# Performance work log

Measured on AMD Instinct MI355X. Metric: run time of the kernel, lower is better.

The kernel has to match this reference:

```python
import jax, jax.numpy as jnp
import numpy as np

D_MODEL = 2048
N_HEADS = 32
N_KV = 8
HEAD_DIM = D_MODEL // N_HEADS  # 64
ROPE_BASE = 500000.0


def _rope_tables(seq_len, dim, dtype):
    inv_freq = 1.0 / (ROPE_BASE ** (jnp.arange(0, dim, 2, dtype=jnp.float32) / dim))
    t = jnp.arange(seq_len, dtype=jnp.float32)
    freqs = jnp.outer(t, inv_freq)          # [S, dim/2]
    emb = jnp.concatenate([freqs, freqs], axis=-1)  # [S, dim]
    return jnp.cos(emb).astype(dtype), jnp.sin(emb).astype(dtype)


def _rotate_half(x):
    x1, x2 = jnp.split(x, 2, axis=-1)
    return jnp.concatenate([-x2, x1], axis=-1)


def setup_inputs() -> dict:
    key = jax.random.key(0)
    ks = jax.random.split(key, 5)
    B, S = 2, 2048
    sc = 0.02
    return {
        "x": jax.random.normal(ks[0], (B, S, D_MODEL), jnp.float32),
        "Wq": jax.random.normal(ks[1], (D_MODEL, N_HEADS * HEAD_DIM), jnp.float32) * sc,
        "Wk": jax.random.normal(ks[2], (D_MODEL, N_KV * HEAD_DIM), jnp.float32) * sc,
        "Wv": jax.random.normal(ks[3], (D_MODEL, N_KV * HEAD_DIM), jnp.float32) * sc,
        "Wo": jax.random.normal(ks[4], (N_HEADS * HEAD_DIM, D_MODEL), jnp.float32) * sc,
    }


def reference(x, Wq, Wk, Wv, Wo):
    B, S, _ = x.shape
    n_rep = N_HEADS // N_KV

    q = (x @ Wq).reshape(B, S, N_HEADS, HEAD_DIM)
    k = (x @ Wk).reshape(B, S, N_KV, HEAD_DIM)
    v = (x @ Wv).reshape(B, S, N_KV, HEAD_DIM)

    cos, sin = _rope_tables(S, HEAD_DIM, x.dtype)
    cos = cos[None, :, None, :]  # [1,S,1,D]
    sin = sin[None, :, None, :]
    q = q * cos + _rotate_half(q) * sin
    k = k * cos + _rotate_half(k) * sin

    # GQA without materializing expanded K/V: group q heads by kv head.
    qg = q.reshape(B, S, N_KV, n_rep, HEAD_DIM)
    scale = 1.0 / jnp.sqrt(jnp.asarray(HEAD_DIM, x.dtype))
    # scores: [B, n_kv, n_rep, Sq, Sk]
    scores = jnp.einsum("bqhrd,bkhd->bhrqk", qg, k) * scale
    attn = jax.nn.softmax(scores, axis=-1)
    out = jnp.einsum("bhrqk,bkhd->bqhrd", attn, v)  # [B,S,n_kv,n_rep,D]
    out = out.reshape(B, S, N_HEADS * HEAD_DIM)
    return out @ Wo
```

## Files before the change

### kernel.cpp

```cpp
#include <hip/hip_runtime.h>
#include <hip/hip_bf16.h>
#include <stdint.h>

#define SS    2048
#define BB    2
#define MT    4096
#define DM    2048
#define NQKVC 3072

typedef __attribute__((ext_vector_type(8))) short s16x8;
typedef __attribute__((ext_vector_type(4))) short s16x4;
typedef __attribute__((ext_vector_type(4))) float f32x4;
typedef __attribute__((ext_vector_type(2))) unsigned u32x2;

typedef __attribute__((address_space(1))) const void* as1cv;
typedef __attribute__((address_space(3))) void* as3v;

__device__ __forceinline__ float b2f(int u) {
  union { unsigned u; float f; } x; x.u = ((unsigned)(u & 0xFFFF)) << 16; return x.f;
}
__device__ __forceinline__ short f2b(float f) {
  union { float f; unsigned u; } x; x.f = f;
  unsigned r = x.u + 0x7FFFu + ((x.u >> 16) & 1u);
  return (short)(r >> 16);
}
__device__ __forceinline__ void gld16(const void* g, void* l) {
  __builtin_amdgcn_global_load_lds((as1cv)(uintptr_t)g, (as3v)(uint32_t)(uintptr_t)l, 16, 0, 0);
}
__device__ __forceinline__ s16x8 ldsfrag(const char* tile, int r, int cb) {
  return *(const s16x8*)(tile + r * 128 + (cb ^ ((r & 7) << 4)));
}
__device__ __forceinline__ f32x4 mfma16(s16x8 a, s16x8 b, f32x4 c) {
  return __builtin_amdgcn_mfma_f32_16x16x32_bf16(a, b, c, 0, 0, 0);
}

__global__ __launch_bounds__(256) void k_xcvt(const float* __restrict__ x,
                                              ushort* __restrict__ xb, int n) {
  int i = (blockIdx.x * 256 + threadIdx.x) * 4;
  if (i >= n) return;
  float4 v = *(const float4*)(x + i);
  s16x4 o = { f2b(v.x), f2b(v.y), f2b(v.z), f2b(v.w) };
  *(s16x4*)(xb + i) = o;
}

__global__ __launch_bounds__(256) void k_rtab(float* __restrict__ rtab) {
  int idx = blockIdx.x * 256 + threadIdx.x;
  int d = idx & 31, s = idx >> 5;
  float invf = exp2f(-(float)d * (18.931568569324174f / 32.0f));
  float sn, c;
  sincosf((float)s * invf, &sn, &c);
  rtab[idx * 2]     = c;
  rtab[idx * 2 + 1] = sn;
}

__global__ __launch_bounds__(256) void k_wt(const float* __restrict__ W,
                                            ushort* __restrict__ out, int N) {
  __shared__ float t[32][33];
  int k0 = blockIdx.x * 32, n0 = blockIdx.y * 32;
  int tx = threadIdx.x & 31, ty = threadIdx.x >> 5;
#pragma unroll
  for (int j = 0; j < 32; j += 8)
    t[ty + j][tx] = W[(size_t)(k0 + ty + j) * N + n0 + tx];
  __syncthreads();
#pragma unroll
  for (int j = 0; j < 32; j += 8)
    out[(size_t)(n0 + ty + j) * 2048 + k0 + tx] = (ushort)f2b(t[tx][ty + j]);
}

__global__ __launch_bounds__(256) void k_vt(const ushort* __restrict__ QKV,
                                            ushort* __restrict__ Vt) {
  __shared__ ushort t[32][33];
  int s0 = blockIdx.x * 32;
  int c0 = (blockIdx.y & 15) * 32;
  int b  = blockIdx.y >> 4;
  int tx = threadIdx.x & 31, ty = threadIdx.x >> 5;
#pragma unroll
  for (int j = 0; j < 32; j += 8)
    t[ty + j][tx] = QKV[(size_t)(b * SS + s0 + ty + j) * NQKVC + 2560 + c0 + tx];
  __syncthreads();
#pragma unroll
  for (int j = 0; j < 32; j += 8)
    Vt[(size_t)(b * 512 + c0 + ty + j) * SS + s0 + tx] = t[tx][ty + j];
}

template <int BF16_OUT, int ROPE>
__global__ __launch_bounds__(256) void k_gemm(const ushort* __restrict__ A,
                                              const ushort* __restrict__ B,
                                              void* __restrict__ Cv,
                                              const float* __restrict__ rtab,
                                              int M, int N, int K) {
  __shared__ __align__(16) char lds[32768];
  char* ldsA = lds;
  char* ldsB = lds + 16384;
  int tid = threadIdx.x, lane = tid & 63, wid = tid >> 6;
  int wr = wid >> 1, wc = wid & 1;
  int row0 = blockIdx.y * 128, col0 = blockIdx.x * 128;
  int fr = lane & 15, fq = lane >> 4;
  f32x4 acc[4][4] = {};
  int rl = lane >> 3;
  int cbs = ((lane & 7) << 4) ^ (rl << 4);
  const char* Ab = (const char*)A;
  const char* Bb = (const char*)B;
  size_t ldb = (size_t)K * 2;

  for (int kt = 0; kt < K; kt += 64) {
#pragma unroll
    for (int i = 0; i < 4; i++) {
      int ra = wid * 32 + i * 8 + rl;
      gld16(Ab + (size_t)(row0 + ra) * ldb + (size_t)kt * 2 + cbs,
            ldsA + (wid * 32 + i * 8) * 128);
      gld16(Bb + (size_t)(col0 + ra) * ldb + (size_t)kt * 2 + cbs,
            ldsB + (wid * 32 + i * 8) * 128);
    }
    __syncthreads();
#pragma unroll
    for (int kk = 0; kk < 2; kk++) {
      int cb = kk * 64 + (fq << 4);
      s16x8 af[4], bg[4];
#pragma unroll
      for (int m = 0; m < 4; m++) af[m] = ldsfrag(ldsA, wr * 64 + m * 16 + fr, cb);
#pragma unroll
      for (int n = 0; n < 4; n++) bg[n] = ldsfrag(ldsB, wc * 64 + n * 16 + fr, cb);
#pragma unroll
      for (int m = 0; m < 4; m++)
#pragma unroll
        for (int n = 0; n < 4; n++)
          acc[m][n] = mfma16(af[m], bg[n], acc[m][n]);
    }
    __syncthreads();
  }

  if (ROPE) {
    int cb0 = col0 + wc * 64;
    if (cb0 < 2560) {
#pragma unroll
      for (int m = 0; m < 4; m++)
#pragma unroll
        for (int i = 0; i < 4; i++) {
          int srow = (row0 + wr * 64 + m * 16 + fq * 4 + i) & (SS - 1);
          const float* tr = rtab + srow * 64;
          float cs0 = tr[fr * 2],        sn0 = tr[fr * 2 + 1];
          float cs1 = tr[32 + fr * 2],   sn1 = tr[32 + fr * 2 + 1];
          float lo0 = acc[m][0][i], hi0 = acc[m][2][i];
          acc[m][0][i] = lo0 * cs0 - hi0 * sn0;
          acc[m][2][i] = hi0 * cs0 + lo0 * sn0;
          float lo1 = acc[m][1][i], hi1 = acc[m][3][i];
          acc[m][1][i] = lo1 * cs1 - hi1 * sn1;
          acc[m][3][i] = hi1 * cs1 + lo1 * sn1;
        }
    }
  }

#pragma unroll
  for (int m = 0; m < 4; m++) {
#pragma unroll
    for (int i = 0; i < 4; i++) {
      int row = row0 + wr * 64 + m * 16 + fq * 4 + i;
      if (BF16_OUT) {
        ushort* C = (ushort*)Cv;
#pragma unroll
        for (int n = 0; n < 4; n++)
          C[(size_t)row * N + col0 + wc * 64 + n * 16 + fr] = (ushort)f2b(acc[m][n][i]);
      } else {
        float* C = (float*)Cv;
#pragma unroll
        for (int n = 0; n < 4; n++)
          C[(size_t)row * N + col0 + wc * 64 + n * 16 + fr] = acc[m][n][i];
      }
    }
  }
}

__global__ __launch_bounds__(256) void k_attn(const ushort* __restrict__ QKV,
                                              const ushort* __restrict__ Vt,
                                              ushort* __restrict__ O) {
  __shared__ __align__(16) char ldsK[16384];
  __shared__ __align__(16) char ldsV[16384];
  __shared__ __align__(16) char ldsP[4][4096];
  int tid = threadIdx.x, lane = tid & 63, wid = tid >> 6;
  int bh = blockIdx.y, b = bh >> 5, h = bh & 31, kv = h >> 2;
  int fr = lane & 15, fq = lane >> 4;
  int q0 = blockIdx.x * 128 + wid * 32;

  const float QSCALE = 0.18033688011112042f;
  s16x8 qf[2][2];
#pragma unroll
  for (int kk = 0; kk < 2; kk++)
#pragma unroll
    for (int qi = 0; qi < 2; qi++) {
      const ushort* src = QKV + (size_t)(b * SS + q0 + qi * 16 + fr) * NQKVC + h * 64 + kk * 32 + fq * 8;
      s16x8 v = *(const s16x8*)src;
#pragma unroll
      for (int j = 0; j < 8; j++) v[j] = f2b(b2f(v[j]) * QSCALE);
      qf[kk][qi] = v;
    }

  const f32x4 fz = {0.f, 0.f, 0.f, 0.f};
  f32x4 o[4][2];
  f32x4 psum[2] = {fz, fz};
#pragma unroll
  for (int n = 0; n < 4; n++) { o[n][0] = fz; o[n][1] = fz; }
  const short ONE = 0x3F80;
  const s16x8 ones = {ONE, ONE, ONE, ONE, ONE, ONE, ONE, ONE};

  int rl = lane >> 3;
  int cbs = ((lane & 7) << 4) ^ (rl << 4);
  const char* Kbase = (const char*)QKV + (size_t)(b * SS) * (NQKVC * 2) + (size_t)(2048 + kv * 64) * 2;
  const char* Vbase = (const char*)Vt + (size_t)((b * 8 + kv) * 64) * (SS * 2);
  char* pw = ldsP[wid];
  int pswz = (fr & 7) << 4;

  for (int t = 0; t < SS / 128; t++) {
#pragma unroll
    for (int j = 0; j < 4; j++) {
      int rr = wid * 32 + j * 8;
      gld16(Kbase + (size_t)(t * 128 + rr + rl) * (NQKVC * 2) + cbs, ldsK + rr * 128);
    }
#pragma unroll
    for (int hh = 0; hh < 2; hh++)
#pragma unroll
      for (int j = 0; j < 2; j++) {
        int rr = wid * 16 + j * 8;
        gld16(Vbase + (size_t)(rr + rl) * (SS * 2) + (size_t)t * 256 + hh * 128 + cbs,
              ldsV + (hh * 64 + rr) * 128);
      }
    __syncthreads();

#pragma unroll
    for (int hh = 0; hh < 2; hh++) {
      const char* Kc = ldsK + hh * 8192;
      const char* Vc = ldsV + hh * 8192;

      f32x4 sf[4][2];
#pragma unroll
      for (int n = 0; n < 4; n++) { sf[n][0] = fz; sf[n][1] = fz; }
#pragma unroll
      for (int kk = 0; kk < 2; kk++) {
        int cb = kk * 64 + (fq << 4);
#pragma unroll
        for (int n = 0; n < 4; n++) {
          s16x8 kf = ldsfrag(Kc, n * 16 + fr, cb);
          sf[n][0] = mfma16(kf, qf[kk][0], sf[n][0]);
          sf[n][1] = mfma16(kf, qf[kk][1], sf[n][1]);
        }
      }

#pragma unroll
      for (int qi = 0; qi < 2; qi++) {
        char* pwr = pw + qi * 2048 + fr * 128;
#pragma unroll
        for (int n = 0; n < 4; n++) {
          float e0 = __builtin_amdgcn_exp2f(sf[n][qi][0]);
          float e1 = __builtin_amdgcn_exp2f(sf[n][qi][1]);
          float e2 = __builtin_amdgcn_exp2f(sf[n][qi][2]);
          float e3 = __builtin_amdgcn_exp2f(sf[n][qi][3]);
          unsigned u01, u23;
          asm("v_cvt_pk_bf16_f32 %0, %1, %2" : "=v"(u01) : "v"(e0), "v"(e1));
          asm("v_cvt_pk_bf16_f32 %0, %1, %2" : "=v"(u23) : "v"(e2), "v"(e3));
          u32x2 w = {u01, u23};
          *(u32x2*)(pwr + ((n * 32 + fq * 8) ^ pswz)) = w;
        }
      }
      asm volatile("" ::: "memory");

#pragma unroll
      for (int kk = 0; kk < 2; kk++) {
        int cb = kk * 64 + (fq << 4);
        s16x8 pa0 = ldsfrag(pw, fr, cb);
        s16x8 pa1 = ldsfrag(pw + 2048, fr, cb);
        psum[0] = mfma16(pa0, ones, psum[0]);
        psum[1] = mfma16(pa1, ones, psum[1]);
#pragma unroll
        for (int n = 0; n < 4; n++) {
          s16x8 vf = ldsfrag(Vc, n * 16 + fr, cb);
          o[n][0] = mfma16(pa0, vf, o[n][0]);
          o[n][1] = mfma16(pa1, vf, o[n][1]);
        }
      }
      asm volatile("" ::: "memory");
    }
    __syncthreads();
  }

#pragma unroll
  for (int qi = 0; qi < 2; qi++) {
    float inv[4];
#pragma unroll
    for (int i = 0; i < 4; i++) inv[i] = 1.0f / psum[qi][i];
#pragma unroll
    for (int n = 0; n < 4; n++) {
      float e0 = o[n][qi][0] * inv[0], e1 = o[n][qi][1] * inv[1];
      float e2 = o[n][qi][2] * inv[2], e3 = o[n][qi][3] * inv[3];
      unsigned u01, u23;
      asm("v_cvt_pk_bf16_f32 %0, %1, %2" : "=v"(u01) : "v"(e0), "v"(e1));
      asm("v_cvt_pk_bf16_f32 %0, %1, %2" : "=v"(u23) : "v"(e2), "v"(e3));
      int colb = n * 32 + fr * 2;
#pragma unroll
      for (int i = 0; i < 4; i++) {
        int r = fq * 4 + i;
        unsigned v16 = (i == 0) ? (u01 & 0xffffu) : (i == 1) ? (u01 >> 16)
                      : (i == 2) ? (u23 & 0xffffu) : (u23 >> 16);
        *(short*)(pw + r * 128 + (colb ^ ((r & 7) << 4))) = (short)v16;
      }
    }
    asm volatile("" ::: "memory");
    int orow = lane >> 2;
    int cbase = (lane & 3) * 32;
    int swo = (orow & 7) << 4;
    s16x8 ov0 = *(const s16x8*)(pw + orow * 128 + (cbase ^ swo));
    s16x8 ov1 = *(const s16x8*)(pw + orow * 128 + ((cbase + 16) ^ swo));
    ushort* dst = O + (size_t)(b * SS + blockIdx.x * 128 + wid * 32 + qi * 16 + orow) * DM + h * 64 + (lane & 3) * 16;
    *(s16x8*)(dst)     = ov0;
    *(s16x8*)(dst + 8) = ov1;
    asm volatile("" ::: "memory");
  }
}

extern "C" void kernel_launch(void* const* d_in, const int* in_sizes, int n_in,
                              void* d_out, int out_size, void* d_ws, size_t ws_size,
                              hipStream_t stream) {
  const float* x  = (const float*)d_in[0];
  const float* Wq = (const float*)d_in[1];
  const float* Wk = (const float*)d_in[2];
  const float* Wv = (const float*)d_in[3];
  const float* Wo = (const float*)d_in[4];
  char* ws = (char*)d_ws;
  ushort* xb    = (ushort*)(ws);
  ushort* Wqkvt = (ushort*)(ws + 16777216);
  ushort* Wot   = (ushort*)(ws + 29360128);
  ushort* QKV   = (ushort*)(ws + 37748736);
  ushort* Vt    = (ushort*)(ws + 62914560);
  ushort* Obuf  = (ushort*)(ws + 67108864);
  float* rtab = (ws_size >= (size_t)83886080 + 524288)
              ? (float*)(ws + 83886080) : (float*)d_out;

  k_xcvt<<<8192, 256, 0, stream>>>(x, xb, MT * DM);
  k_rtab<<<256, 256, 0, stream>>>(rtab);
  k_wt<<<dim3(64, 64), 256, 0, stream>>>(Wq, Wqkvt, 2048);
  k_wt<<<dim3(64, 16), 256, 0, stream>>>(Wk, Wqkvt + (size_t)2048 * 2048, 512);
  k_wt<<<dim3(64, 16), 256, 0, stream>>>(Wv, Wqkvt + (size_t)2560 * 2048, 512);
  k_wt<<<dim3(64, 64), 256, 0, stream>>>(Wo, Wot, 2048);
  k_gemm<1, 1><<<dim3(24, 32), 256, 0, stream>>>(xb, Wqkvt, (void*)QKV, rtab, MT, NQKVC, DM);
  k_vt<<<dim3(64, 32), 256, 0, stream>>>(QKV, Vt);
  k_attn<<<dim3(16, 64), 256, 0, stream>>>(QKV, Vt, Obuf);
  k_gemm<0, 0><<<dim3(16, 32), 256, 0, stream>>>(Obuf, Wot, d_out, nullptr, MT, DM, DM);
}
```

Baseline: 254.0 us.

## Merge weight prep launches, swizzle block order for XCDs, halve attention P buffer

Five preprocessing launches (four weight transposes plus the RoPE table) are merged into one kernel that dispatches on block index, cutting launch overhead. GEMM and attention blocks are remapped with a mod-8 swizzle so that neighbouring tiles land on the same XCD and share L2. The attention kernel processes its two 16-row query halves one at a time through a P buffer half the previous size, which lowers LDS use and may raise occupancy but serialises the P write/read per half.

```diff
diff --git a/kernel.cpp b/kernel.cpp
--- a/kernel.cpp
+++ b/kernel.cpp
@@ -32,6 +32,14 @@
 }
 __device__ __forceinline__ f32x4 mfma16(s16x8 a, s16x8 b, f32x4 c) {
   return __builtin_amdgcn_mfma_f32_16x16x32_bf16(a, b, c, 0, 0, 0);
+}
+__device__ __forceinline__ void swz8(int& bx, int& by) {
+  int gx = gridDim.x;
+  int lin = by * gx + bx;
+  int tot = gx * gridDim.y;
+  int s = (lin & 7) * (tot >> 3) + (lin >> 3);
+  bx = s % gx;
+  by = s / gx;
 }
 
 __global__ __launch_bounds__(256) void k_xcvt(const float* __restrict__ x,
@@ -43,20 +51,31 @@
   *(s16x4*)(xb + i) = o;
 }
 
-__global__ __launch_bounds__(256) void k_rtab(float* __restrict__ rtab) {
-  int idx = blockIdx.x * 256 + threadIdx.x;
-  int d = idx & 31, s = idx >> 5;
-  float invf = exp2f(-(float)d * (18.931568569324174f / 32.0f));
-  float sn, c;
-  sincosf((float)s * invf, &sn, &c);
-  rtab[idx * 2]     = c;
-  rtab[idx * 2 + 1] = sn;
-}
-
-__global__ __launch_bounds__(256) void k_wt(const float* __restrict__ W,
-                                            ushort* __restrict__ out, int N) {
+__global__ __launch_bounds__(256) void k_wpre(const float* __restrict__ Wq,
+                                              const float* __restrict__ Wk,
+                                              const float* __restrict__ Wv,
+                                              const float* __restrict__ Wo,
+                                              ushort* __restrict__ Wqkvt,
+                                              ushort* __restrict__ Wot,
+                                              float* __restrict__ rtab) {
   __shared__ float t[32][33];
-  int k0 = blockIdx.x * 32, n0 = blockIdx.y * 32;
+  int bid = blockIdx.x;
+  if (bid >= 10240) {
+    int idx = (bid - 10240) * 256 + threadIdx.x;
+    int d = idx & 31, s = idx >> 5;
+    float invf = exp2f(-(float)d * (18.931568569324174f / 32.0f));
+    float sn, c;
+    sincosf((float)s * invf, &sn, &c);
+    rtab[idx * 2]     = c;
+    rtab[idx * 2 + 1] = sn;
+    return;
+  }
+  const float* W; ushort* out; int N; int l;
+  if (bid < 4096)      { W = Wq; out = Wqkvt;                         N = 2048; l = bid; }
+  else if (bid < 5120) { W = Wk; out = Wqkvt + (size_t)2048 * 2048;   N = 512;  l = bid - 4096; }
+  else if (bid < 6144) { W = Wv; out = Wqkvt + (size_t)2560 * 2048;   N = 512;  l = bid - 5120; }
+  else                 { W = Wo; out = Wot;                           N = 2048; l = bid - 6144; }
+  int k0 = (l & 63) * 32, n0 = (l >> 6) * 32;
   int tx = threadIdx.x & 31, ty = threadIdx.x >> 5;
 #pragma unroll
   for (int j = 0; j < 32; j += 8)
@@ -92,9 +111,11 @@
   __shared__ __align__(16) char lds[32768];
   char* ldsA = lds;
   char* ldsB = lds + 16384;
+  int bx = blockIdx.x, by = blockIdx.y;
+  swz8(bx, by);
   int tid = threadIdx.x, lane = tid & 63, wid = tid >> 6;
   int wr = wid >> 1, wc = wid & 1;
-  int row0 = blockIdx.y * 128, col0 = blockIdx.x * 128;
+  int row0 = by * 128, col0 = bx * 128;
   int fr = lane & 15, fq = lane >> 4;
   f32x4 acc[4][4] = {};
   int rl = lane >> 3;
@@ -176,11 +197,13 @@
                                               ushort* __restrict__ O) {
   __shared__ __align__(16) char ldsK[16384];
   __shared__ __align__(16) char ldsV[16384];
-  __shared__ __align__(16) char ldsP[4][4096];
+  __shared__ __align__(16) char ldsP[4][2048];
+  int bx = blockIdx.x, by = blockIdx.y;
+  swz8(bx, by);
   int tid = threadIdx.x, lane = tid & 63, wid = tid >> 6;
-  int bh = blockIdx.y, b = bh >> 5, h = bh & 31, kv = h >> 2;
+  int bh = by, b = bh >> 5, h = bh & 31, kv = h >> 2;
   int fr = lane & 15, fq = lane >> 4;
-  int q0 = blockIdx.x * 128 + wid * 32;
+  int q0 = bx * 128 + wid * 32;
 
   const float QSCALE = 0.18033688011112042f;
   s16x8 qf[2][2];
@@ -247,7 +270,7 @@
 
 #pragma unroll
       for (int qi = 0; qi < 2; qi++) {
-        char* pwr = pw + qi * 2048 + fr * 128;
+        char* pwr = pw + fr * 128;
 #pragma unroll
         for (int n = 0; n < 4; n++) {
           float e0 = __builtin_amdgcn_exp2f(sf[n][qi][0]);
@@ -260,24 +283,20 @@
           u32x2 w = {u01, u23};
           *(u32x2*)(pwr + ((n * 32 + fq * 8) ^ pswz)) = w;
         }
-      }
-      asm volatile("" ::: "memory");
-
-#pragma unroll
-      for (int kk = 0; kk < 2; kk++) {
-        int cb = kk * 64 + (fq << 4);
-        s16x8 pa0 = ldsfrag(pw, fr, cb);
-        s16x8 pa1 = ldsfrag(pw + 2048, fr, cb);
-        psum[0] = mfma16(pa0, ones, psum[0]);
-        psum[1] = mfma16(pa1, ones, psum[1]);
-#pragma unroll
-        for (int n = 0; n < 4; n++) {
-          s16x8 vf = ldsfrag(Vc, n * 16 + fr, cb);
-          o[n][0] = mfma16(pa0, vf, o[n][0]);
-          o[n][1] = mfma16(pa1, vf, o[n][1]);
+        asm volatile("" ::: "memory");
+#pragma unroll
+        for (int kk = 0; kk < 2; kk++) {
+          int cb = kk * 64 + (fq << 4);
+          s16x8 pa = ldsfrag(pw, fr, cb);
+          psum[qi] = mfma16(pa, ones, psum[qi]);
+#pragma unroll
+          for (int n = 0; n < 4; n++) {
+            s16x8 vf = ldsfrag(Vc, n * 16 + fr, cb);
+            o[n][qi] = mfma16(pa, vf, o[n][qi]);
+          }
         }
-      }
-      asm volatile("" ::: "memory");
+        asm volatile("" ::: "memory");
+      }
     }
     __syncthreads();
   }
@@ -309,7 +328,7 @@
     int swo = (orow & 7) << 4;
     s16x8 ov0 = *(const s16x8*)(pw + orow * 128 + (cbase ^ swo));
     s16x8 ov1 = *(const s16x8*)(pw + orow * 128 + ((cbase + 16) ^ swo));
-    ushort* dst = O + (size_t)(b * SS + blockIdx.x * 128 + wid * 32 + qi * 16 + orow) * DM + h * 64 + (lane & 3) * 16;
+    ushort* dst = O + (size_t)(b * SS + bx * 128 + wid * 32 + qi * 16 + orow) * DM + h * 64 + (lane & 3) * 16;
     *(s16x8*)(dst)     = ov0;
     *(s16x8*)(dst + 8) = ov1;
     asm volatile("" ::: "memory");
@@ -335,11 +354,7 @@
               ? (float*)(ws + 83886080) : (float*)d_out;
 
   k_xcvt<<<8192, 256, 0, stream>>>(x, xb, MT * DM);
-  k_rtab<<<256, 256, 0, stream>>>(rtab);
-  k_wt<<<dim3(64, 64), 256, 0, stream>>>(Wq, Wqkvt, 2048);
-  k_wt<<<dim3(64, 16), 256, 0, stream>>>(Wk, Wqkvt + (size_t)2048 * 2048, 512);
-  k_wt<<<dim3(64, 16), 256, 0, stream>>>(Wv, Wqkvt + (size_t)2560 * 2048, 512);
-  k_wt<<<dim3(64, 64), 256, 0, stream>>>(Wo, Wot, 2048);
+  k_wpre<<<10496, 256, 0, stream>>>(Wq, Wk, Wv, Wo, Wqkvt, Wot, rtab);
   k_gemm<1, 1><<<dim3(24, 32), 256, 0, stream>>>(xb, Wqkvt, (void*)QKV, rtab, MT, NQKVC, DM);
   k_vt<<<dim3(64, 32), 256, 0, stream>>>(QKV, Vt);
   k_attn<<<dim3(16, 64), 256, 0, stream>>>(QKV, Vt, Obuf);
```

After: 245.9 us. 1.03x faster.
